# Performance work log

Measured on AMD Instinct MI355X. Metric: run time of the kernel, lower is better.

## Reference

```python
import jax, jax.numpy as jnp
import numpy as np

NUM_HEADS = 8
WS = 8
NORM_FAC = 1.0 / 200.0


def _sine_pe(coords, dim):
    # coords: [P, 2] with channels (x, y); FlowFormer LinearPositionEmbeddingSine
    nf = dim // 4
    freq = jnp.arange(nf, dtype=jnp.float32)  # linspace(0, nf-1, nf)
    px = 3.14 * coords[..., 0:1] * freq * NORM_FAC
    py = 3.14 * coords[..., 1:2] * freq * NORM_FAC
    return jnp.concatenate([jnp.sin(px), jnp.cos(px), jnp.sin(py), jnp.cos(py)], axis=-1)


def setup_inputs() -> dict:
    key = jax.random.key(0)
    ks = jax.random.split(key, 10)
    B, H, W, C = 8, 128, 128, 256
    x = jax.random.normal(ks[0], (B, H * W, C), dtype=jnp.float32)
    wscale = 0.05
    inp = {"x": x}
    for i, nm in enumerate(["q", "k", "v", "p"]):
        inp[f"W_{nm}"] = jax.random.normal(ks[1 + 2 * i], (C, C), dtype=jnp.float32) * wscale
        inp[f"b_{nm}"] = jax.random.normal(ks[2 + 2 * i], (C,), dtype=jnp.float32) * wscale
    inp["H"] = H
    inp["W"] = W
    return inp


def reference(x, W_q, b_q, W_k, b_k, W_v, b_v, W_p, b_p, H, W):
    B, N, C = x.shape
    nh, ws = NUM_HEADS, WS
    hd = C // nh
    scale = hd ** -0.5
    xg = x.reshape(B, H, W, C)
    pad_b = (-H) % ws
    pad_r = (-W) % ws
    xg = jnp.pad(xg, ((0, 0), (0, pad_b), (0, pad_r), (0, 0)))
    Hp, Wp = H + pad_b, W + pad_r
    h, w = Hp // ws, Wp // ws
    # [B, h, w, ws, ws, C] windows
    xw = xg.reshape(B, h, ws, w, ws, C).transpose(0, 1, 3, 2, 4, 5)
    # v is computed BEFORE adding the positional encoding (as in the original)
    v = xw @ W_v.T + b_v
    # sinusoidal RPE on window coordinates (same for every window)
    ys, xs = jnp.meshgrid(jnp.arange(ws, dtype=jnp.float32), jnp.arange(ws, dtype=jnp.float32), indexing="ij")
    coords = jnp.stack([xs, ys], axis=-1).reshape(-1, 2)  # [ws*ws, 2] (x, y)
    pe = _sine_pe(coords, C).reshape(ws, ws, C)
    xw = xw + pe[None, None, None]
    q = xw @ W_q.T + b_q
    k = xw @ W_k.T + b_k

    def to_heads(t):  # -> [B, h*w, nh, ws*ws, hd]
        return t.reshape(B, h * w, ws * ws, nh, hd).transpose(0, 1, 3, 2, 4)

    q, k, v = to_heads(q), to_heads(k), to_heads(v)
    attn = jax.nn.softmax(jnp.einsum("bgnpd,bgnqd->bgnpq", q, k) * scale, axis=-1)
    o = jnp.einsum("bgnpq,bgnqd->bgnpd", attn, v)
    o = o.transpose(0, 1, 3, 2, 4).reshape(B, h, w, ws, ws, C)
    o = o.transpose(0, 1, 3, 2, 4, 5).reshape(B, Hp, Wp, C)[:, :H, :W]
    return o.reshape(B, N, C) @ W_p.T + b_p
```

## Files before the change

### kernel.cpp

```cpp
#include <hip/hip_runtime.h>

typedef __bf16 bf16x8 __attribute__((ext_vector_type(8)));
typedef float f32x4 __attribute__((ext_vector_type(4)));

#define MFMA16(a, b, c) __builtin_amdgcn_mfma_f32_16x16x32_bf16((a), (b), (c), 0, 0, 0)
#define LDS_FENCE() __asm__ volatile("s_waitcnt lgkmcnt(0)" ::: "memory")

__device__ __forceinline__ unsigned short f2bf(float f) {
    union { float f; unsigned int u; } v;
    v.f = f;
    unsigned int r = v.u + 0x7fffu + ((v.u >> 16) & 1u);
    return (unsigned short)(r >> 16);
}

__global__ __launch_bounds__(256) void cvt_weights(
    const float* __restrict__ Wq, const float* __restrict__ Wk,
    const float* __restrict__ Wv, const float* __restrict__ Wp,
    unsigned short* __restrict__ out)
{
    int i = blockIdx.x * 256 + threadIdx.x;
    out[i]          = f2bf(Wq[i]);
    out[65536 + i]  = f2bf(Wk[i]);
    out[131072 + i] = f2bf(Wv[i]);
    out[196608 + i] = f2bf(Wp[i]);
}

__global__ __launch_bounds__(256) void pe_bias(
    const float* __restrict__ Wq, const float* __restrict__ bq,
    const float* __restrict__ Wk, const float* __restrict__ bk,
    float* __restrict__ qpe, float* __restrict__ kpe)
{
    __shared__ float pet[8 * 260];
    const int tid = threadIdx.x;
    for (int i = tid; i < 8 * 256; i += 256) {
        int v = i >> 8, k = i & 255;
        float ang = 3.14f * (float)v * (float)(k & 63) * 0.005f;
        pet[v * 260 + k] = (k & 64) ? __cosf(ang) : __sinf(ang);
    }
    __syncthreads();

    const int p = tid & 63;
    const int c = blockIdx.x * 4 + (tid >> 6);
    const int jx = p & 7, iy = p >> 3;
    const float* rq = Wq + (size_t)c * 256;
    const float* rk = Wk + (size_t)c * 256;
    const float* pl = pet + jx * 260;
    const float* ph = pet + iy * 260;
    float aq = bq[c], ak = bk[c];
    #pragma unroll 8
    for (int k = 0; k < 128; ++k) { float pv = pl[k]; aq += pv * rq[k]; ak += pv * rk[k]; }
    #pragma unroll 8
    for (int k = 128; k < 256; ++k) { float pv = ph[k]; aq += pv * rq[k]; ak += pv * rk[k]; }
    qpe[p * 256 + c] = aq;
    kpe[p * 256 + c] = ak;
}

#define STRX 264
#define STRV 72
#define STRS 40

__global__ __launch_bounds__(512, 4) void fused_attn(
    const float* __restrict__ x,
    const unsigned short* __restrict__ Wall,
    const float* __restrict__ bv,
    const float* __restrict__ qpe,
    const float* __restrict__ kpe,
    const float* __restrict__ bp,
    float* __restrict__ out)
{
    __shared__ unsigned short sm[38912];
    unsigned short* xs = sm;
    unsigned short* vs = sm + 20480;
    unsigned short* os = sm + 20480;

    const int tid  = threadIdx.x;
    const int w    = tid >> 6;
    const int lane = tid & 63;
    const int quad = lane >> 4;
    const int l15  = lane & 15;
    unsigned short* scr = sm + w * 2560;

    const int g = blockIdx.x;
    const int b = g >> 8, wy = (g >> 4) & 15, wx = g & 15;
    const int rowbase = b * 16384 + wy * 1024 + wx * 8;

    const f32x4 zero4 = {0.f, 0.f, 0.f, 0.f};

    {
        const int tk = tid >> 3;
        const int c0 = (tid & 7) * 32;
        const int gr = rowbase + (tk >> 3) * 128 + (tk & 7);
        const float* xr = x + (size_t)gr * 256 + c0;
        #pragma unroll
        for (int i = 0; i < 32; i += 8) {
            float4 f0 = *(const float4*)(xr + i);
            float4 f1 = *(const float4*)(xr + i + 4);
            alignas(16) unsigned short st[8] = {
                f2bf(f0.x), f2bf(f0.y), f2bf(f0.z), f2bf(f0.w),
                f2bf(f1.x), f2bf(f1.y), f2bf(f1.z), f2bf(f1.w)};
            *(uint4*)&xs[tk * STRX + c0 + i] = *(const uint4*)st;
        }
    }
    __syncthreads();

    {
        const unsigned short* Wv = Wall + 131072;
        f32x4 acc[2][4];
        #pragma unroll
        for (int i = 0; i < 2; ++i)
            #pragma unroll
            for (int j = 0; j < 4; ++j) acc[i][j] = zero4;
        #pragma unroll 2
        for (int k0 = 0; k0 < 256; k0 += 32) {
            bf16x8 a[2], bb[4];
            #pragma unroll
            for (int i = 0; i < 2; ++i)
                a[i] = *(const bf16x8*)&Wv[(size_t)(w * 32 + i * 16 + l15) * 256 + k0 + quad * 8];
            #pragma unroll
            for (int j = 0; j < 4; ++j)
                bb[j] = *(const bf16x8*)&xs[(j * 16 + l15) * STRX + k0 + quad * 8];
            #pragma unroll
            for (int i = 0; i < 2; ++i)
                #pragma unroll
                for (int j = 0; j < 4; ++j)
                    acc[i][j] = MFMA16(a[i], bb[j], acc[i][j]);
        }
        #pragma unroll
        for (int i = 0; i < 2; ++i) {
            #pragma unroll
            for (int r = 0; r < 4; ++r) {
                const int c = w * 32 + i * 16 + quad * 4 + r;
                const float bbv = bv[c];
                #pragma unroll
                for (int j = 0; j < 4; ++j)
                    vs[c * STRV + j * 16 + l15] = f2bf(acc[i][j][r] + bbv);
            }
        }
    }

    f32x4 aq[4][2], ak[4][2];
    {
        const unsigned short* Wq = Wall;
        const unsigned short* Wk = Wall + 65536;
        #pragma unroll
        for (int i = 0; i < 4; ++i)
            #pragma unroll
            for (int j = 0; j < 2; ++j) { aq[i][j] = zero4; ak[i][j] = zero4; }
        #pragma unroll 2
        for (int k0 = 0; k0 < 256; k0 += 32) {
            bf16x8 af[4], bq[2], bk[2];
            #pragma unroll
            for (int i = 0; i < 4; ++i)
                af[i] = *(const bf16x8*)&xs[(i * 16 + l15) * STRX + k0 + quad * 8];
            #pragma unroll
            for (int j = 0; j < 2; ++j) {
                bq[j] = *(const bf16x8*)&Wq[(size_t)(w * 32 + j * 16 + l15) * 256 + k0 + quad * 8];
                bk[j] = *(const bf16x8*)&Wk[(size_t)(w * 32 + j * 16 + l15) * 256 + k0 + quad * 8];
            }
            #pragma unroll
            for (int i = 0; i < 4; ++i)
                #pragma unroll
                for (int j = 0; j < 2; ++j) {
                    aq[i][j] = MFMA16(af[i], bq[j], aq[i][j]);
                    ak[i][j] = MFMA16(af[i], bk[j], ak[i][j]);
                }
        }
    }
    __syncthreads();

    f32x4 oa[4][2];
    {
        #pragma unroll
        for (int i = 0; i < 4; ++i)
            #pragma unroll
            for (int r = 0; r < 4; ++r) {
                const int m = i * 16 + quad * 4 + r;
                #pragma unroll
                for (int j = 0; j < 2; ++j) {
                    const int n = w * 32 + j * 16 + l15;
                    scr[m * STRS + j * 16 + l15] = f2bf(aq[i][j][r] + qpe[m * 256 + n]);
                }
            }
        LDS_FENCE();
        bf16x8 fq[4];
        #pragma unroll
        for (int t = 0; t < 4; ++t)
            fq[t] = *(const bf16x8*)&scr[(t * 16 + l15) * STRS + quad * 8];
        LDS_FENCE();
        #pragma unroll
        for (int i = 0; i < 4; ++i)
            #pragma unroll
            for (int r = 0; r < 4; ++r) {
                const int m = i * 16 + quad * 4 + r;
                #pragma unroll
                for (int j = 0; j < 2; ++j) {
                    const int n = w * 32 + j * 16 + l15;
                    scr[m * STRS + j * 16 + l15] = f2bf(ak[i][j][r] + kpe[m * 256 + n]);
                }
            }
        LDS_FENCE();
        bf16x8 fk[4];
        #pragma unroll
        for (int t = 0; t < 4; ++t)
            fk[t] = *(const bf16x8*)&scr[(t * 16 + l15) * STRS + quad * 8];

        f32x4 s[4][4];
        #pragma unroll
        for (int mt = 0; mt < 4; ++mt)
            #pragma unroll
            for (int nt = 0; nt < 4; ++nt)
                s[mt][nt] = MFMA16(fq[mt], fk[nt], zero4);

        const float KF = 0.17677669529663687f * 1.4426950408889634f;
        #pragma unroll
        for (int mt = 0; mt < 4; ++mt) {
            #pragma unroll
            for (int r = 0; r < 4; ++r) {
                float mx = fmaxf(fmaxf(s[mt][0][r], s[mt][1][r]), fmaxf(s[mt][2][r], s[mt][3][r]));
                #pragma unroll
                for (int off = 1; off < 16; off <<= 1) mx = fmaxf(mx, __shfl_xor(mx, off, 16));
                float e[4];
                float sum = 0.f;
                #pragma unroll
                for (int nt = 0; nt < 4; ++nt) { e[nt] = exp2f((s[mt][nt][r] - mx) * KF); sum += e[nt]; }
                #pragma unroll
                for (int off = 1; off < 16; off <<= 1) sum += __shfl_xor(sum, off, 16);
                const float inv = 1.0f / sum;
                #pragma unroll
                for (int nt = 0; nt < 4; ++nt) s[mt][nt][r] = e[nt] * inv;
            }
        }

        #pragma unroll
        for (int mt = 0; mt < 4; ++mt) { oa[mt][0] = zero4; oa[mt][1] = zero4; }
        #pragma unroll
        for (int kt = 0; kt < 2; ++kt) {
            LDS_FENCE();
            #pragma unroll
            for (int mt = 0; mt < 4; ++mt)
                #pragma unroll
                for (int r = 0; r < 4; ++r) {
                    const int row = mt * 16 + quad * 4 + r;
                    #pragma unroll
                    for (int nt2 = 0; nt2 < 2; ++nt2)
                        scr[row * STRS + nt2 * 16 + l15] = f2bf(s[mt][kt * 2 + nt2][r]);
                }
            LDS_FENCE();
            bf16x8 ap[4], bvf[2];
            #pragma unroll
            for (int mt = 0; mt < 4; ++mt)
                ap[mt] = *(const bf16x8*)&scr[(mt * 16 + l15) * STRS + quad * 8];
            #pragma unroll
            for (int nv = 0; nv < 2; ++nv)
                bvf[nv] = *(const bf16x8*)&vs[(w * 32 + nv * 16 + l15) * STRV + kt * 32 + quad * 8];
            #pragma unroll
            for (int mt = 0; mt < 4; ++mt)
                #pragma unroll
                for (int nv = 0; nv < 2; ++nv)
                    oa[mt][nv] = MFMA16(ap[mt], bvf[nv], oa[mt][nv]);
        }
    }
    __syncthreads();

    #pragma unroll
    for (int mt = 0; mt < 4; ++mt)
        #pragma unroll
        for (int r = 0; r < 4; ++r) {
            const int m = mt * 16 + quad * 4 + r;
            #pragma unroll
            for (int nv = 0; nv < 2; ++nv)
                os[m * STRX + w * 32 + nv * 16 + l15] = f2bf(oa[mt][nv][r]);
        }
    __syncthreads();

    {
        const unsigned short* Wp = Wall + 196608;
        f32x4 ac[4][2];
        #pragma unroll
        for (int i = 0; i < 4; ++i) { ac[i][0] = zero4; ac[i][1] = zero4; }
        #pragma unroll 2
        for (int k0 = 0; k0 < 256; k0 += 32) {
            bf16x8 af[4], bb[2];
            #pragma unroll
            for (int i = 0; i < 4; ++i)
                af[i] = *(const bf16x8*)&os[(i * 16 + l15) * STRX + k0 + quad * 8];
            #pragma unroll
            for (int j = 0; j < 2; ++j)
                bb[j] = *(const bf16x8*)&Wp[(size_t)(w * 32 + j * 16 + l15) * 256 + k0 + quad * 8];
            #pragma unroll
            for (int i = 0; i < 4; ++i)
                #pragma unroll
                for (int j = 0; j < 2; ++j)
                    ac[i][j] = MFMA16(af[i], bb[j], ac[i][j]);
        }
        #pragma unroll
        for (int j = 0; j < 2; ++j) {
            const int n = w * 32 + j * 16 + l15;
            const float bbp = bp[n];
            #pragma unroll
            for (int i = 0; i < 4; ++i) {
                #pragma unroll
                for (int r = 0; r < 4; ++r) {
                    const int m = i * 16 + quad * 4 + r;
                    const int gr = rowbase + (m >> 3) * 128 + (m & 7);
                    out[(size_t)gr * 256 + n] = ac[i][j][r] + bbp;
                }
            }
        }
    }
}

extern "C" void kernel_launch(void* const* d_in, const int* in_sizes, int n_in,
                              void* d_out, int out_size, void* d_ws, size_t ws_size,
                              hipStream_t stream) {
    const float* x  = (const float*)d_in[0];
    const float* Wq = (const float*)d_in[1];
    const float* bq = (const float*)d_in[2];
    const float* Wk = (const float*)d_in[3];
    const float* bk = (const float*)d_in[4];
    const float* Wv = (const float*)d_in[5];
    const float* bv = (const float*)d_in[6];
    const float* Wp = (const float*)d_in[7];
    const float* bp = (const float*)d_in[8];
    float* out = (float*)d_out;

    char* ws = (char*)d_ws;
    unsigned short* Wbf = (unsigned short*)ws;
    float* qpe = (float*)(ws + 524288);
    float* kpe = (float*)(ws + 524288 + 65536);

    cvt_weights<<<256, 256, 0, stream>>>(Wq, Wk, Wv, Wp, Wbf);
    pe_bias<<<64, 256, 0, stream>>>(Wq, bq, Wk, bk, qpe, kpe);
    fused_attn<<<2048, 512, 0, stream>>>(x, Wbf, bv, qpe, kpe, bp, out);
}
```

Measured before the change: 386.0 us.

## Keep attention fragments in registers via transposed MFMA layouts, merge prep kernels

Computes Q/K projections and the P·V product in transposed form so MFMA output fragments can be repacked directly into operand fragments in registers. This removes the per-wave LDS scratch round trips and their lgkmcnt fences, along with one block-wide barrier. The positional-bias tables are stored transposed to match the new fragment layout, and the V store now packs four values per write. The two preprocessing kernels are merged into one launch, and LDS usage shrinks, which may allow more blocks per CU at the cost of more register repacking work.

```diff
diff --git a/kernel.cpp b/kernel.cpp
--- a/kernel.cpp
+++ b/kernel.cpp
@@ -4,7 +4,6 @@
 typedef float f32x4 __attribute__((ext_vector_type(4)));
 
 #define MFMA16(a, b, c) __builtin_amdgcn_mfma_f32_16x16x32_bf16((a), (b), (c), 0, 0, 0)
-#define LDS_FENCE() __asm__ volatile("s_waitcnt lgkmcnt(0)" ::: "memory")
 
 __device__ __forceinline__ unsigned short f2bf(float f) {
     union { float f; unsigned int u; } v;
@@ -13,72 +12,78 @@
     return (unsigned short)(r >> 16);
 }
 
-__global__ __launch_bounds__(256) void cvt_weights(
-    const float* __restrict__ Wq, const float* __restrict__ Wk,
-    const float* __restrict__ Wv, const float* __restrict__ Wp,
-    unsigned short* __restrict__ out)
-{
-    int i = blockIdx.x * 256 + threadIdx.x;
-    out[i]          = f2bf(Wq[i]);
-    out[65536 + i]  = f2bf(Wk[i]);
-    out[131072 + i] = f2bf(Wv[i]);
-    out[196608 + i] = f2bf(Wp[i]);
-}
-
-__global__ __launch_bounds__(256) void pe_bias(
+__global__ __launch_bounds__(256) void prep(
     const float* __restrict__ Wq, const float* __restrict__ bq,
     const float* __restrict__ Wk, const float* __restrict__ bk,
-    float* __restrict__ qpe, float* __restrict__ kpe)
+    const float* __restrict__ Wv, const float* __restrict__ Wp,
+    unsigned short* __restrict__ Wbf,
+    float* __restrict__ qpeT, float* __restrict__ kpeT)
 {
-    __shared__ float pet[8 * 260];
     const int tid = threadIdx.x;
-    for (int i = tid; i < 8 * 256; i += 256) {
-        int v = i >> 8, k = i & 255;
+    {
+        int i = blockIdx.x * 256 + tid;
+        Wbf[i]          = f2bf(Wq[i]);
+        Wbf[65536 + i]  = f2bf(Wk[i]);
+        Wbf[131072 + i] = f2bf(Wv[i]);
+        Wbf[196608 + i] = f2bf(Wp[i]);
+    }
+    if (blockIdx.x >= 64) return;
+
+    __shared__ float pet[8 * 264];
+    for (int t = tid; t < 8 * 256; t += 256) {
+        int v = t >> 8, k = t & 255;
         float ang = 3.14f * (float)v * (float)(k & 63) * 0.005f;
-        pet[v * 260 + k] = (k & 64) ? __cosf(ang) : __sinf(ang);
+        pet[v * 264 + k] = (k & 64) ? __cosf(ang) : __sinf(ang);
     }
     __syncthreads();
 
     const int p = tid & 63;
     const int c = blockIdx.x * 4 + (tid >> 6);
     const int jx = p & 7, iy = p >> 3;
-    const float* rq = Wq + (size_t)c * 256;
-    const float* rk = Wk + (size_t)c * 256;
-    const float* pl = pet + jx * 260;
-    const float* ph = pet + iy * 260;
+    const float4* rq4 = (const float4*)(Wq + (size_t)c * 256);
+    const float4* rk4 = (const float4*)(Wk + (size_t)c * 256);
+    const float4* pl4 = (const float4*)(pet + jx * 264);
+    const float4* ph4 = (const float4*)(pet + iy * 264);
     float aq = bq[c], ak = bk[c];
     #pragma unroll 8
-    for (int k = 0; k < 128; ++k) { float pv = pl[k]; aq += pv * rq[k]; ak += pv * rk[k]; }
+    for (int t = 0; t < 32; ++t) {
+        float4 pv = pl4[t], wq = rq4[t], wk = rk4[t];
+        aq += pv.x * wq.x + pv.y * wq.y + pv.z * wq.z + pv.w * wq.w;
+        ak += pv.x * wk.x + pv.y * wk.y + pv.z * wk.z + pv.w * wk.w;
+    }
     #pragma unroll 8
-    for (int k = 128; k < 256; ++k) { float pv = ph[k]; aq += pv * rq[k]; ak += pv * rk[k]; }
-    qpe[p * 256 + c] = aq;
-    kpe[p * 256 + c] = ak;
+    for (int t = 0; t < 32; ++t) {
+        float4 pv = ph4[t], wq = rq4[32 + t], wk = rk4[32 + t];
+        aq += pv.x * wq.x + pv.y * wq.y + pv.z * wq.z + pv.w * wq.w;
+        ak += pv.x * wk.x + pv.y * wk.y + pv.z * wk.z + pv.w * wk.w;
+    }
+    qpeT[c * 64 + p] = aq;
+    kpeT[c * 64 + p] = ak;
 }
 
 #define STRX 264
 #define STRV 72
-#define STRS 40
+#define VSOFF 16896
 
 __global__ __launch_bounds__(512, 4) void fused_attn(
     const float* __restrict__ x,
     const unsigned short* __restrict__ Wall,
     const float* __restrict__ bv,
-    const float* __restrict__ qpe,
-    const float* __restrict__ kpe,
+    const float* __restrict__ qpeT,
+    const float* __restrict__ kpeT,
     const float* __restrict__ bp,
     float* __restrict__ out)
 {
-    __shared__ unsigned short sm[38912];
+    __shared__ unsigned short sm[35328];
     unsigned short* xs = sm;
-    unsigned short* vs = sm + 20480;
-    unsigned short* os = sm + 20480;
+    unsigned short* vs = sm + VSOFF;
+    unsigned short* os = sm + VSOFF;
 
     const int tid  = threadIdx.x;
     const int w    = tid >> 6;
     const int lane = tid & 63;
     const int quad = lane >> 4;
     const int l15  = lane & 15;
-    unsigned short* scr = sm + w * 2560;
 
     const int g = blockIdx.x;
     const int b = g >> 8, wy = (g >> 4) & 15, wx = g & 15;
@@ -105,35 +110,34 @@
 
     {
         const unsigned short* Wv = Wall + 131072;
-        f32x4 acc[2][4];
-        #pragma unroll
-        for (int i = 0; i < 2; ++i)
-            #pragma unroll
-            for (int j = 0; j < 4; ++j) acc[i][j] = zero4;
+        f32x4 acc[4][2];
+        #pragma unroll
+        for (int i = 0; i < 4; ++i) { acc[i][0] = zero4; acc[i][1] = zero4; }
         #pragma unroll 2
         for (int k0 = 0; k0 < 256; k0 += 32) {
-            bf16x8 a[2], bb[4];
-            #pragma unroll
-            for (int i = 0; i < 2; ++i)
-                a[i] = *(const bf16x8*)&Wv[(size_t)(w * 32 + i * 16 + l15) * 256 + k0 + quad * 8];
-            #pragma unroll
-            for (int j = 0; j < 4; ++j)
-                bb[j] = *(const bf16x8*)&xs[(j * 16 + l15) * STRX + k0 + quad * 8];
-            #pragma unroll
-            for (int i = 0; i < 2; ++i)
-                #pragma unroll
-                for (int j = 0; j < 4; ++j)
-                    acc[i][j] = MFMA16(a[i], bb[j], acc[i][j]);
-        }
-        #pragma unroll
-        for (int i = 0; i < 2; ++i) {
-            #pragma unroll
-            for (int r = 0; r < 4; ++r) {
-                const int c = w * 32 + i * 16 + quad * 4 + r;
-                const float bbv = bv[c];
-                #pragma unroll
-                for (int j = 0; j < 4; ++j)
-                    vs[c * STRV + j * 16 + l15] = f2bf(acc[i][j][r] + bbv);
+            bf16x8 af[4], wv[2];
+            #pragma unroll
+            for (int i = 0; i < 4; ++i)
+                af[i] = *(const bf16x8*)&xs[(i * 16 + l15) * STRX + k0 + quad * 8];
+            #pragma unroll
+            for (int j = 0; j < 2; ++j)
+                wv[j] = *(const bf16x8*)&Wv[(size_t)(w * 32 + j * 16 + l15) * 256 + k0 + quad * 8];
+            #pragma unroll
+            for (int i = 0; i < 4; ++i)
+                #pragma unroll
+                for (int j = 0; j < 2; ++j)
+                    acc[i][j] = MFMA16(af[i], wv[j], acc[i][j]);
+        }
+        #pragma unroll
+        for (int j = 0; j < 2; ++j) {
+            const int ch = w * 32 + j * 16 + l15;
+            const float bbv = bv[ch];
+            #pragma unroll
+            for (int i = 0; i < 4; ++i) {
+                alignas(8) unsigned short t4[4];
+                #pragma unroll
+                for (int r = 0; r < 4; ++r) t4[r] = f2bf(acc[i][j][r] + bbv);
+                *(uint2*)&vs[ch * STRV + i * 16 + quad * 4] = *(const uint2*)t4;
             }
         }
     }
@@ -148,116 +152,107 @@
             for (int j = 0; j < 2; ++j) { aq[i][j] = zero4; ak[i][j] = zero4; }
         #pragma unroll 2
         for (int k0 = 0; k0 < 256; k0 += 32) {
-            bf16x8 af[4], bq[2], bk[2];
+            bf16x8 af[4], wq[2], wk[2];
             #pragma unroll
             for (int i = 0; i < 4; ++i)
                 af[i] = *(const bf16x8*)&xs[(i * 16 + l15) * STRX + k0 + quad * 8];
             #pragma unroll
             for (int j = 0; j < 2; ++j) {
-                bq[j] = *(const bf16x8*)&Wq[(size_t)(w * 32 + j * 16 + l15) * 256 + k0 + quad * 8];
-                bk[j] = *(const bf16x8*)&Wk[(size_t)(w * 32 + j * 16 + l15) * 256 + k0 + quad * 8];
+                wq[j] = *(const bf16x8*)&Wq[(size_t)(w * 32 + j * 16 + l15) * 256 + k0 + quad * 8];
+                wk[j] = *(const bf16x8*)&Wk[(size_t)(w * 32 + j * 16 + l15) * 256 + k0 + quad * 8];
             }
             #pragma unroll
             for (int i = 0; i < 4; ++i)
                 #pragma unroll
                 for (int j = 0; j < 2; ++j) {
-                    aq[i][j] = MFMA16(af[i], bq[j], aq[i][j]);
-                    ak[i][j] = MFMA16(af[i], bk[j], ak[i][j]);
+                    aq[i][j] = MFMA16(wq[j], af[i], aq[i][j]);
+                    ak[i][j] = MFMA16(wk[j], af[i], ak[i][j]);
                 }
         }
     }
-    __syncthreads();
-
-    f32x4 oa[4][2];
-    {
-        #pragma unroll
-        for (int i = 0; i < 4; ++i)
-            #pragma unroll
-            for (int r = 0; r < 4; ++r) {
-                const int m = i * 16 + quad * 4 + r;
-                #pragma unroll
-                for (int j = 0; j < 2; ++j) {
-                    const int n = w * 32 + j * 16 + l15;
-                    scr[m * STRS + j * 16 + l15] = f2bf(aq[i][j][r] + qpe[m * 256 + n]);
+
+    f32x4 oaT[2][4];
+    {
+        const float* qb = qpeT + (size_t)(w * 32 + quad * 4) * 64 + l15;
+        const float* kb = kpeT + (size_t)(w * 32 + quad * 4) * 64 + l15;
+        bf16x8 fq[4], fk[4];
+        #pragma unroll
+        for (int i = 0; i < 4; ++i) {
+            alignas(16) unsigned short tq[8], tk8[8];
+            #pragma unroll
+            for (int e = 0; e < 8; ++e) {
+                const int j = e >> 2, r = e & 3;
+                const int off = (j * 16 + r) * 64 + i * 16;
+                tq[e]  = f2bf(aq[i][j][r] + qb[off]);
+                tk8[e] = f2bf(ak[i][j][r] + kb[off]);
+            }
+            fq[i] = *(const bf16x8*)tq;
+            fk[i] = *(const bf16x8*)tk8;
+        }
+
+        f32x4 s[4][4];
+        #pragma unroll
+        for (int pt = 0; pt < 4; ++pt)
+            #pragma unroll
+            for (int mt = 0; mt < 4; ++mt)
+                s[pt][mt] = MFMA16(fk[pt], fq[mt], zero4);
+
+        const float KF = 0.17677669529663687f * 1.4426950408889634f;
+        #pragma unroll
+        for (int mt = 0; mt < 4; ++mt) {
+            float mx = s[0][mt][0];
+            #pragma unroll
+            for (int pt = 0; pt < 4; ++pt)
+                #pragma unroll
+                for (int r = 0; r < 4; ++r) mx = fmaxf(mx, s[pt][mt][r]);
+            mx = fmaxf(mx, __shfl_xor(mx, 16));
+            mx = fmaxf(mx, __shfl_xor(mx, 32));
+            float sum = 0.f;
+            #pragma unroll
+            for (int pt = 0; pt < 4; ++pt)
+                #pragma unroll
+                for (int r = 0; r < 4; ++r) {
+                    float e = exp2f((s[pt][mt][r] - mx) * KF);
+                    s[pt][mt][r] = e;
+                    sum += e;
                 }
-            }
-        LDS_FENCE();
-        bf16x8 fq[4];
-        #pragma unroll
-        for (int t = 0; t < 4; ++t)
-            fq[t] = *(const bf16x8*)&scr[(t * 16 + l15) * STRS + quad * 8];
-        LDS_FENCE();
-        #pragma unroll
-        for (int i = 0; i < 4; ++i)
-            #pragma unroll
-            for (int r = 0; r < 4; ++r) {
-                const int m = i * 16 + quad * 4 + r;
-                #pragma unroll
-                for (int j = 0; j < 2; ++j) {
-                    const int n = w * 32 + j * 16 + l15;
-                    scr[m * STRS + j * 16 + l15] = f2bf(ak[i][j][r] + kpe[m * 256 + n]);
-                }
-            }
-        LDS_FENCE();
-        bf16x8 fk[4];
-        #pragma unroll
-        for (int t = 0; t < 4; ++t)
-            fk[t] = *(const bf16x8*)&scr[(t * 16 + l15) * STRS + quad * 8];
-
-        f32x4 s[4][4];
-        #pragma unroll
-        for (int mt = 0; mt < 4; ++mt)
-            #pragma unroll
-            for (int nt = 0; nt < 4; ++nt)
-                s[mt][nt] = MFMA16(fq[mt], fk[nt], zero4);
-
-        const float KF = 0.17677669529663687f * 1.4426950408889634f;
-        #pragma unroll
-        for (int mt = 0; mt < 4; ++mt) {
-            #pragma unroll
-            for (int r = 0; r < 4; ++r) {
-                float mx = fmaxf(fmaxf(s[mt][0][r], s[mt][1][r]), fmaxf(s[mt][2][r], s[mt][3][r]));
-                #pragma unroll
-                for (int off = 1; off < 16; off <<= 1) mx = fmaxf(mx, __shfl_xor(mx, off, 16));
-                float e[4];
-                float sum = 0.f;
-                #pragma unroll
-                for (int nt = 0; nt < 4; ++nt) { e[nt] = exp2f((s[mt][nt][r] - mx) * KF); sum += e[nt]; }
-                #pragma unroll
-                for (int off = 1; off < 16; off <<= 1) sum += __shfl_xor(sum, off, 16);
-                const float inv = 1.0f / sum;
-                #pragma unroll
-                for (int nt = 0; nt < 4; ++nt) s[mt][nt][r] = e[nt] * inv;
-            }
-        }
-
-        #pragma unroll
-        for (int mt = 0; mt < 4; ++mt) { oa[mt][0] = zero4; oa[mt][1] = zero4; }
+            sum += __shfl_xor(sum, 16);
+            sum += __shfl_xor(sum, 32);
+            const float inv = 1.0f / sum;
+            #pragma unroll
+            for (int pt = 0; pt < 4; ++pt)
+                #pragma unroll
+                for (int r = 0; r < 4; ++r) s[pt][mt][r] *= inv;
+        }
+
+        #pragma unroll
+        for (int nv = 0; nv < 2; ++nv)
+            #pragma unroll
+            for (int mt = 0; mt < 4; ++mt) oaT[nv][mt] = zero4;
         #pragma unroll
         for (int kt = 0; kt < 2; ++kt) {
-            LDS_FENCE();
-            #pragma unroll
-            for (int mt = 0; mt < 4; ++mt)
-                #pragma unroll
-                for (int r = 0; r < 4; ++r) {
-                    const int row = mt * 16 + quad * 4 + r;
-                    #pragma unroll
-                    for (int nt2 = 0; nt2 < 2; ++nt2)
-                        scr[row * STRS + nt2 * 16 + l15] = f2bf(s[mt][kt * 2 + nt2][r]);
-                }
-            LDS_FENCE();
-            bf16x8 ap[4], bvf[2];
-            #pragma unroll
-            for (int mt = 0; mt < 4; ++mt)
-                ap[mt] = *(const bf16x8*)&scr[(mt * 16 + l15) * STRS + quad * 8];
+            bf16x8 pf[4], vf[2];
+            #pragma unroll
+            for (int mt = 0; mt < 4; ++mt) {
+                alignas(16) unsigned short t8[8];
+                #pragma unroll
+                for (int e = 0; e < 8; ++e)
+                    t8[e] = f2bf(s[kt * 2 + (e >> 2)][mt][e & 3]);
+                pf[mt] = *(const bf16x8*)t8;
+            }
+            #pragma unroll
+            for (int nv = 0; nv < 2; ++nv) {
+                const int c = w * 32 + nv * 16 + l15;
+                alignas(16) unsigned short t8[8];
+                *(uint2*)&t8[0] = *(const uint2*)&vs[c * STRV + kt * 32 + quad * 4];
+                *(uint2*)&t8[4] = *(const uint2*)&vs[c * STRV + kt * 32 + 16 + quad * 4];
+                vf[nv] = *(const bf16x8*)t8;
+            }
             #pragma unroll
             for (int nv = 0; nv < 2; ++nv)
-                bvf[nv] = *(const bf16x8*)&vs[(w * 32 + nv * 16 + l15) * STRV + kt * 32 + quad * 8];
-            #pragma unroll
-            for (int mt = 0; mt < 4; ++mt)
-                #pragma unroll
-                for (int nv = 0; nv < 2; ++nv)
-                    oa[mt][nv] = MFMA16(ap[mt], bvf[nv], oa[mt][nv]);
+                #pragma unroll
+                for (int mt = 0; mt < 4; ++mt)
+                    oaT[nv][mt] = MFMA16(vf[nv], pf[mt], oaT[nv][mt]);
         }
     }
     __syncthreads();
@@ -265,11 +260,11 @@
     #pragma unroll
     for (int mt = 0; mt < 4; ++mt)
         #pragma unroll
-        for (int r = 0; r < 4; ++r) {
-            const int m = mt * 16 + quad * 4 + r;
-            #pragma unroll
-            for (int nv = 0; nv < 2; ++nv)
-                os[m * STRX + w * 32 + nv * 16 + l15] = f2bf(oa[mt][nv][r]);
+        for (int nv = 0; nv < 2; ++nv) {
+            alignas(8) unsigned short t4[4];
+            #pragma unroll
+            for (int r = 0; r < 4; ++r) t4[r] = f2bf(oaT[nv][mt][r]);
+            *(uint2*)&os[(mt * 16 + l15) * STRX + w * 32 + nv * 16 + quad * 4] = *(const uint2*)t4;
         }
     __syncthreads();
 
@@ -326,10 +321,9 @@
 
     char* ws = (char*)d_ws;
     unsigned short* Wbf = (unsigned short*)ws;
-    float* qpe = (float*)(ws + 524288);
-    float* kpe = (float*)(ws + 524288 + 65536);
-
-    cvt_weights<<<256, 256, 0, stream>>>(Wq, Wk, Wv, Wp, Wbf);
-    pe_bias<<<64, 256, 0, stream>>>(Wq, bq, Wk, bk, qpe, kpe);
-    fused_attn<<<2048, 512, 0, stream>>>(x, Wbf, bv, qpe, kpe, bp, out);
+    float* qpeT = (float*)(ws + 524288);
+    float* kpeT = (float*)(ws + 524288 + 65536);
+
+    prep<<<256, 256, 0, stream>>>(Wq, bq, Wk, bk, Wv, Wp, Wbf, qpeT, kpeT);
+    fused_attn<<<2048, 512, 0, stream>>>(x, Wbf, bv, qpeT, kpeT, bp, out);
 }
```

New measurement: 367.2 us. 1.05x faster.
